# Kernel tuning notes

Hardware: AMD Instinct MI355X
Metric: run time of the kernel (lower is better)

The kernel has to match this reference:

```python
import jax, jax.numpy as jnp
import numpy as np

B, S, D, H = 2, 2048, 1024, 16
HD = D // H  # head_dim = 64


def setup_inputs() -> dict:
    key = jax.random.key(0)
    ks = jax.random.split(key, 12)
    sc = 1.0 / np.sqrt(D)
    return {
        "query": jax.random.normal(ks[0], (B, S, D), jnp.float32),
        "key_": jax.random.normal(ks[1], (B, S, D), jnp.float32),
        "value": jax.random.normal(ks[2], (B, S, D), jnp.float32),
        "mask": jax.random.randint(ks[3], (B, 1, S, S), 0, 2, jnp.int32),
        "Wq": jax.random.normal(ks[4], (D, D), jnp.float32) * sc,
        "bq": jnp.zeros((D,), jnp.float32),
        "Wk": jax.random.normal(ks[5], (D, D), jnp.float32) * sc,
        "bk": jnp.zeros((D,), jnp.float32),
        "Wv": jax.random.normal(ks[6], (D, D), jnp.float32) * sc,
        "bv": jnp.zeros((D,), jnp.float32),
        "Wo": jax.random.normal(ks[7], (D, D), jnp.float32) * sc,
        "bo": jnp.zeros((D,), jnp.float32),
    }


def _split(x):
    # [B, S, D] -> [B, H, S, HD]
    return x.reshape(B, S, H, HD).transpose(0, 2, 1, 3)


def reference(query, key_, value, mask, Wq, bq, Wk, bk, Wv, bv, Wo, bo):
    Q = _split(query @ Wq + bq)
    K = _split(key_ @ Wk + bk)
    V = _split(value @ Wv + bv)
    # scores: [B, H, Sq, Sk]
    scores = jnp.einsum("bhqd,bhkd->bhqk", Q, K) / jnp.sqrt(jnp.float32(HD))
    scores = jnp.where(mask == 0, jnp.float32(-1e9), scores)
    probs = jax.nn.softmax(scores, axis=-1)
    attn = jnp.einsum("bhqk,bhkd->bhqd", probs, V)
    out = attn.transpose(0, 2, 1, 3).reshape(B, S, D)
    return out @ Wo + bo
```

## Files before the change

### kernel.cpp

```cpp
#include <hip/hip_runtime.h>
#include <stdint.h>

typedef _Float16 f16;
typedef _Float16 f16x4 __attribute__((ext_vector_type(4)));
typedef _Float16 f16x8 __attribute__((ext_vector_type(8)));
typedef __fp16 hf16x2 __attribute__((ext_vector_type(2)));
typedef float f32x4 __attribute__((ext_vector_type(4)));
typedef float f32x16 __attribute__((ext_vector_type(16)));
typedef unsigned u32;
typedef unsigned uint2v __attribute__((ext_vector_type(2)));

static constexpr int Bb = 2, Ss = 2048, Dd = 1024, Hh = 16, HDd = 64;
static constexpr int M_ROWS = Bb * Ss;

static constexpr size_t OFF_WT  = 24ull << 20;
static constexpr size_t OFF_QKV = 32ull << 20;
static constexpr size_t OFF_ATT = 56ull << 20;
static constexpr size_t OFF_MB  = 64ull << 20;

__device__ __forceinline__ void gll16(const void* g, void* l) {
  __builtin_amdgcn_global_load_lds((__attribute__((address_space(1))) const void*)g,
                                   (__attribute__((address_space(3))) void*)l, 16, 0, 0);
}

__device__ __forceinline__ int lds_byte(int row, int slot) {
  return row * 128 + (((slot ^ (row & 7)) & 7) << 4);
}

__device__ __forceinline__ float ex2(float x) {
  float r; asm("v_exp_f32 %0, %1" : "=v"(r) : "v"(x)); return r;
}

union H2U { hf16x2 h; u32 u; };

__global__ __launch_bounds__(256) void prep(const int* __restrict__ mask,
                                            unsigned* __restrict__ bits,
                                            const float* __restrict__ wq,
                                            const float* __restrict__ wk,
                                            const float* __restrict__ wv,
                                            const float* __restrict__ wo,
                                            f16* __restrict__ wt) {
  const int bid = blockIdx.x;
  __shared__ float t[32][33];
  if (bid < 32768) {
    size_t i = (size_t)bid * 256 + threadIdx.x;
    int v = mask[i];
    unsigned long long bm = __ballot(v != 0);
    if ((threadIdx.x & 63) == 0) {
      size_t w = i >> 5;
      bits[w]     = (unsigned)bm;
      bits[w + 1] = (unsigned)(bm >> 32);
    }
  } else {
    const int wb = bid - 32768;
    const int z = wb >> 10, by = (wb >> 5) & 31, bx = wb & 31;
    const float* W = z == 0 ? wq : z == 1 ? wk : z == 2 ? wv : wo;
    f16* Wt = wt + (size_t)z * Dd * Dd;
    const int tx = threadIdx.x & 31, ty = threadIdx.x >> 5;
    const int k0 = by * 32, n0 = bx * 32;
    for (int i = 0; i < 32; i += 8) t[ty + i][tx] = W[(size_t)(k0 + ty + i) * Dd + n0 + tx];
    __syncthreads();
    for (int i = 0; i < 32; i += 8) Wt[(size_t)(n0 + ty + i) * Dd + k0 + tx] = (f16)t[tx][ty + i];
  }
}

__global__ __launch_bounds__(256) void gemm_qkv(const float* __restrict__ qin,
                                                const float* __restrict__ kin,
                                                const float* __restrict__ vin,
                                                const f16* __restrict__ Btbase,
                                                const float* __restrict__ b0,
                                                const float* __restrict__ b1,
                                                const float* __restrict__ b2,
                                                f16* __restrict__ Cbase) {
  constexpr int K = Dd, N = Dd;
  const int f = blockIdx.x;
  const int z = f >> 8, i = f & 255;
  const int xg = i & 7, sl = i >> 3;
  const int m0 = (xg * 4 + (sl >> 3)) * 128, n0 = (sl & 7) * 128;
  const float* A = z == 0 ? qin : z == 1 ? kin : vin;
  const f16* Bt = Btbase + (size_t)z * N * K;
  const float* bias = z == 0 ? b0 : z == 1 ? b1 : b2;

  __shared__ char smem[81920];
  const int tid = threadIdx.x, l = tid & 63, w = tid >> 6;
  const int li = l & 15, gq = l >> 4;
  const int wm = (w >> 1) * 64, wn = (w & 1) * 64;
  const int sr = l >> 3, ss = l & 7;
  const int scol = ((ss ^ sr) << 3);

  f32x4 acc[4][4];
  for (int mi = 0; mi < 4; mi++)
    for (int ni = 0; ni < 4; ni++) acc[mi][ni] = f32x4{0.f, 0.f, 0.f, 0.f};

  float4 a0[2][4], a1[2][4];

#pragma unroll
  for (int t = 0; t < 2; t++) {
    const int kt = t * 64;
#pragma unroll
    for (int c = 0; c < 4; c++) {
      int chunk = w * 4 + c, r = chunk * 8 + sr;
      gll16(Bt + (size_t)(n0 + r) * K + kt + scol, smem + 32768 + t * 16384 + chunk * 1024);
      const float* src = A + (size_t)(m0 + r) * K + kt + scol;
      a0[t][c] = *(const float4*)src;
      a1[t][c] = *(const float4*)(src + 4);
    }
  }

#pragma unroll
  for (int t = 0; t < 16; t++) {
    if (t < 15) asm volatile("s_waitcnt vmcnt(12)" ::: "memory");
    else        asm volatile("s_waitcnt vmcnt(0)"  ::: "memory");

    {
      char* bufA = smem + (t & 1) * 16384;
#pragma unroll
      for (int c = 0; c < 4; c++) {
        int chunk = w * 4 + c;
        H2U h0, h1, h2, h3;
        h0.h = __builtin_amdgcn_cvt_pkrtz(a0[t & 1][c].x, a0[t & 1][c].y);
        h1.h = __builtin_amdgcn_cvt_pkrtz(a0[t & 1][c].z, a0[t & 1][c].w);
        h2.h = __builtin_amdgcn_cvt_pkrtz(a1[t & 1][c].x, a1[t & 1][c].y);
        h3.h = __builtin_amdgcn_cvt_pkrtz(a1[t & 1][c].z, a1[t & 1][c].w);
        union { u32 uu[4]; f16x8 v8; } pk;
        pk.uu[0] = h0.u; pk.uu[1] = h1.u; pk.uu[2] = h2.u; pk.uu[3] = h3.u;
        *(f16x8*)(bufA + chunk * 1024 + l * 16) = pk.v8;
      }
    }
    asm volatile("s_waitcnt lgkmcnt(0)" ::: "memory");
    __builtin_amdgcn_s_barrier();

    if (t + 2 < 16) {
      const int tn = t + 2, kn = tn * 64;
#pragma unroll
      for (int c = 0; c < 4; c++) {
        int chunk = w * 4 + c, r = chunk * 8 + sr;
        gll16(Bt + (size_t)(n0 + r) * K + kn + scol,
              smem + 32768 + (tn % 3) * 16384 + chunk * 1024);
        const float* src = A + (size_t)(m0 + r) * K + kn + scol;
        a0[tn & 1][c] = *(const float4*)src;
        a1[tn & 1][c] = *(const float4*)(src + 4);
      }
    }
    __builtin_amdgcn_sched_barrier(0);

    const char* Asc = smem + (t & 1) * 16384;
    const char* Bsc = smem + 32768 + (t % 3) * 16384;
#pragma unroll
    for (int ks = 0; ks < 2; ks++) {
      f16x8 af[4], bf[4];
#pragma unroll
      for (int ii = 0; ii < 4; ii++) {
        af[ii] = *(const f16x8*)(Asc + lds_byte(wm + ii * 16 + li, ks * 4 + gq));
        bf[ii] = *(const f16x8*)(Bsc + lds_byte(wn + ii * 16 + li, ks * 4 + gq));
      }
#pragma unroll
      for (int mi = 0; mi < 4; mi++)
#pragma unroll
        for (int ni = 0; ni < 4; ni++)
          acc[mi][ni] = __builtin_amdgcn_mfma_f32_16x16x32_f16(af[mi], bf[ni], acc[mi][ni], 0, 0, 0);
    }
  }

  const float scl = (z == 0) ? 0.18033688011112042f : 1.0f;
  if (z == 2) {
    f16* Vt = Cbase + (size_t)2 * M_ROWS * N;
#pragma unroll
    for (int mi = 0; mi < 4; mi++)
#pragma unroll
      for (int ni = 0; ni < 4; ni++) {
        const int col = n0 + wn + ni * 16 + li;
        const int r0  = m0 + wm + mi * 16 + gq * 4;
        const int bb_ = r0 >> 11, s = r0 & 2047;
        const float bv = bias[col];
        f16x4 pk;
#pragma unroll
        for (int j = 0; j < 4; j++) pk[j] = (f16)(acc[mi][ni][j] + bv);
        *(f16x4*)(Vt + ((size_t)(bb_ * Hh) << 17) + (size_t)col * Ss + s) = pk;
      }
  } else {
    for (int mi = 0; mi < 4; mi++)
      for (int ni = 0; ni < 4; ni++) {
        const int r0  = m0 + wm + mi * 16 + gq * 4;
        const int col = n0 + wn + ni * 16 + li;
        const float bb = bias[col];
#pragma unroll
        for (int j = 0; j < 4; j++) {
          float val = (acc[mi][ni][j] + bb) * scl;
          Cbase[(size_t)z * M_ROWS * N + (size_t)(r0 + j) * N + col] = (f16)val;
        }
      }
  }
}

__global__ __launch_bounds__(256) void gemm_out(const f16* __restrict__ A,
                                                const f16* __restrict__ Bt,
                                                const float* __restrict__ bias,
                                                float* __restrict__ C) {
  constexpr int K = Dd, N = Dd;
  const int f = blockIdx.x;
  const int xg = f & 7, sl = f >> 3;
  const int m0 = (xg * 4 + (sl >> 3)) * 128, n0 = (sl & 7) * 128;
  __shared__ char smem[65536];
  const int tid = threadIdx.x, l = tid & 63, w = tid >> 6;
  const int li = l & 15, gq = l >> 4;
  const int wm = (w >> 1) * 64, wn = (w & 1) * 64;
  const int sr = l >> 3, ss = l & 7;
  const int scol = ((ss ^ sr) << 3);

  f32x4 acc[4][4];
  for (int mi = 0; mi < 4; mi++)
    for (int ni = 0; ni < 4; ni++) acc[mi][ni] = f32x4{0.f, 0.f, 0.f, 0.f};

#pragma unroll
  for (int c = 0; c < 4; c++) {
    int chunk = w * 4 + c, r = chunk * 8 + sr;
    gll16(A  + (size_t)(m0 + r) * K + scol, smem + chunk * 1024);
    gll16(Bt + (size_t)(n0 + r) * K + scol, smem + 16384 + chunk * 1024);
  }

  int cur = 0;
  for (int it = 0; it < 16; it++) {
    __syncthreads();
    char* Asc = smem + cur * 32768;
    char* Bsc = Asc + 16384;
    if (it < 15) {
      char* Asn = smem + (cur ^ 1) * 32768;
      const int kn = (it + 1) * 64;
#pragma unroll
      for (int c = 0; c < 4; c++) {
        int chunk = w * 4 + c, r = chunk * 8 + sr;
        gll16(A  + (size_t)(m0 + r) * K + kn + scol, Asn + chunk * 1024);
        gll16(Bt + (size_t)(n0 + r) * K + kn + scol, Asn + 16384 + chunk * 1024);
      }
    }
#pragma unroll
    for (int ks = 0; ks < 2; ks++) {
      f16x8 af[4], bf[4];
#pragma unroll
      for (int ii = 0; ii < 4; ii++) {
        af[ii] = *(const f16x8*)(Asc + lds_byte(wm + ii * 16 + li, ks * 4 + gq));
        bf[ii] = *(const f16x8*)(Bsc + lds_byte(wn + ii * 16 + li, ks * 4 + gq));
      }
#pragma unroll
      for (int mi = 0; mi < 4; mi++)
#pragma unroll
        for (int ni = 0; ni < 4; ni++)
          acc[mi][ni] = __builtin_amdgcn_mfma_f32_16x16x32_f16(af[mi], bf[ni], acc[mi][ni], 0, 0, 0);
    }
    cur ^= 1;
  }

  for (int mi = 0; mi < 4; mi++)
    for (int ni = 0; ni < 4; ni++) {
      const int r0  = m0 + wm + mi * 16 + gq * 4;
      const int col = n0 + wn + ni * 16 + li;
      const float bb = bias[col];
#pragma unroll
      for (int j = 0; j < 4; j++)
        C[(size_t)(r0 + j) * N + col] = acc[mi][ni][j] + bb;
    }
}

__global__ __launch_bounds__(512, 4) void attn_fused(const f16* __restrict__ Qp,
                                                     const f16* __restrict__ Kp,
                                                     const f16* __restrict__ Vt,
                                                     const u32* __restrict__ mbits,
                                                     f16* __restrict__ outp) {
  const int flat = blockIdx.x;
  const int xcd = flat & 7, jj = flat >> 3;
  const int qt = jj & 15;
  const int hb = xcd * 4 + (jj >> 4);
  const int h = hb & 15, b = hb >> 4;

  const int tid = threadIdx.x, l = tid & 63, w = tid >> 6;
  const int lo = l & 31, hi = l >> 5;
  const int half = w >> 2, wsub = w & 3;
  const int q0 = qt * 128, wq = wsub * 32;

  __shared__ char smem[65536];
  char* hbase = smem + half * 32768;
  char* Qst = smem + 16384;

  const size_t qkbase = (size_t)b * Ss * Dd + (size_t)h * HDd;
  const f16* Vtb = Vt + (size_t)(b * Hh + h) * HDd * Ss;
  const int sr = l >> 3, ss = l & 7;
  const int scol = ((ss ^ sr) << 3);

  for (int c = 0; c < 2; c++) {
    int chunk = w * 2 + c, r = chunk * 8 + sr;
    gll16(Qp + qkbase + (size_t)(q0 + r) * Dd + scol, Qst + chunk * 1024);
  }
  const int kt0 = half * 16;
  for (int c = 0; c < 2; c++) {
    int chunk = wsub * 2 + c, r = chunk * 8 + sr;
    gll16(Kp + qkbase + (size_t)(kt0 * 64 + r) * Dd + scol, hbase + chunk * 1024);
    gll16(Vtb + (size_t)r * Ss + kt0 * 64 + scol, hbase + 8192 + chunk * 1024);
  }
  __syncthreads();

  f16x8 qf[4];
#pragma unroll
  for (int c = 0; c < 4; c++)
    qf[c] = *(const f16x8*)(Qst + lds_byte(wq + lo, 2 * c + hi));
  __syncthreads();

  f32x16 accO0 = {0}, accO1 = {0};
  float m_run = -1e30f, l_run = 0.f;
  const u32* mrow = mbits + (size_t)(b * Ss + q0 + wq + lo) * 64;

  for (int it = 0; it < 16; it++) {
    const int kt = kt0 + it;
    if (it) __syncthreads();
    char* bufc = hbase + (it & 1) * 16384;
    if (it < 15) {
      char* bufn = hbase + ((it + 1) & 1) * 16384;
      const int k0n = (kt + 1) * 64;
      for (int c = 0; c < 2; c++) {
        int chunk = wsub * 2 + c, r = chunk * 8 + sr;
        gll16(Kp + qkbase + (size_t)(k0n + r) * Dd + scol, bufn + chunk * 1024);
        gll16(Vtb + (size_t)r * Ss + k0n + scol, bufn + 8192 + chunk * 1024);
      }
    }
    const char* Kb = bufc;
    const char* Vb = bufc + 8192;

    f32x16 s0 = {0}, s1 = {0};
    __builtin_amdgcn_s_setprio(1);
#pragma unroll
    for (int c = 0; c < 4; c++) {
      f16x8 kf0 = *(const f16x8*)(Kb + lds_byte(lo, 2 * c + hi));
      f16x8 kf1 = *(const f16x8*)(Kb + lds_byte(32 + lo, 2 * c + hi));
      s0 = __builtin_amdgcn_mfma_f32_32x32x16_f16(kf0, qf[c], s0, 0, 0, 0);
      s1 = __builtin_amdgcn_mfma_f32_32x32x16_f16(kf1, qf[c], s1, 0, 0, 0);
    }
    __builtin_amdgcn_s_setprio(0);

    uint2v mw = *(const uint2v*)(mrow + kt * 2);
    u32 wa = mw.x >> (hi << 2);
    u32 wb = mw.y >> (hi << 2);

    float x0 = fmaxf(s0[0], s1[0]), x1 = fmaxf(s0[1], s1[1]);
    float x2 = fmaxf(s0[2], s1[2]), x3 = fmaxf(s0[3], s1[3]);
#pragma unroll
    for (int r = 4; r < 16; r += 4) {
      x0 = fmaxf(x0, fmaxf(s0[r],     s1[r]));
      x1 = fmaxf(x1, fmaxf(s0[r + 1], s1[r + 1]));
      x2 = fmaxf(x2, fmaxf(s0[r + 2], s1[r + 2]));
      x3 = fmaxf(x3, fmaxf(s0[r + 3], s1[r + 3]));
    }
    float pm = fmaxf(fmaxf(x0, x1), fmaxf(x2, x3));

    float mn;
    if (__all(pm <= m_run + 11.5f)) {
      mn = m_run;
    } else {
      pm = fmaxf(pm, __shfl_xor(pm, 32));
      mn = fmaxf(m_run, pm);
      const float so = ex2(m_run - mn);
      m_run = mn;
      l_run *= so;
      accO0 *= so; accO1 *= so;
    }

    float racc = 0.f;
#pragma unroll
    for (int r = 0; r < 16; r++) {
      const int kk = (r & 3) + 8 * (r >> 2);
      u32 ma = (u32)(((int)(wa << (31 - kk))) >> 31);
      u32 mb = (u32)(((int)(wb << (31 - kk))) >> 31);
      float e0 = __uint_as_float(__float_as_uint(ex2(s0[r] - mn)) & ma);
      float e1 = __uint_as_float(__float_as_uint(ex2(s1[r] - mn)) & mb);
      s0[r] = e0; s1[r] = e1;
      racc += e0 + e1;
    }
    l_run += racc;

    u32 pw[16];
#pragma unroll
    for (int j = 0; j < 8; j++) {
      H2U a, c;
      a.h = __builtin_amdgcn_cvt_pkrtz(s0[2 * j], s0[2 * j + 1]);
      c.h = __builtin_amdgcn_cvt_pkrtz(s1[2 * j], s1[2 * j + 1]);
      pw[j] = a.u; pw[8 + j] = c.u;
    }
#pragma unroll
    for (int c = 0; c < 4; c++) {
      asm volatile("v_permlane32_swap_b32 %0, %1" : "+v"(pw[4 * c]), "+v"(pw[4 * c + 2]));
      asm volatile("v_permlane32_swap_b32 %0, %1" : "+v"(pw[4 * c + 1]), "+v"(pw[4 * c + 3]));
    }

    __builtin_amdgcn_s_setprio(1);
#pragma unroll
    for (int c = 0; c < 4; c++) {
      union { u32 u[4]; f16x8 v; } pu;
      pu.u[0] = pw[4 * c]; pu.u[1] = pw[4 * c + 1];
      pu.u[2] = pw[4 * c + 2]; pu.u[3] = pw[4 * c + 3];
      f16x8 vf0 = *(const f16x8*)(Vb + lds_byte(lo, 2 * c + hi));
      f16x8 vf1 = *(const f16x8*)(Vb + lds_byte(32 + lo, 2 * c + hi));
      accO0 = __builtin_amdgcn_mfma_f32_32x32x16_f16(vf0, pu.v, accO0, 0, 0, 0);
      accO1 = __builtin_amdgcn_mfma_f32_32x32x16_f16(vf1, pu.v, accO1, 0, 0, 0);
    }
    __builtin_amdgcn_s_setprio(0);
  }

  __syncthreads();
  float* mg = (float*)smem;
  if (half == 1) {
    float* p = mg + (size_t)(wsub * 64 + l) * 35;
#pragma unroll
    for (int r = 0; r < 16; r++) { p[r] = accO0[r]; p[16 + r] = accO1[r]; }
    p[32] = m_run; p[33] = l_run;
  }
  __syncthreads();
  if (half == 1) return;

  const float* p = mg + (size_t)(wsub * 64 + l) * 35;
  const float mB = p[32], lB = p[33];
  const float m = fmaxf(m_run, mB);
  const float fA = ex2(m_run - m), fB = ex2(mB - m);
  float lmerged = l_run * fA + lB * fB;
#pragma unroll
  for (int r = 0; r < 16; r++) {
    accO0[r] = accO0[r] * fA + p[r] * fB;
    accO1[r] = accO1[r] * fA + p[16 + r] * fB;
  }
  const float lf = lmerged + __shfl_xor(lmerged, 32);
  const float inv = 1.0f / lf;

  char* Ot = smem + 40960 + wsub * 4096;
#pragma unroll
  for (int j = 0; j < 8; j++) {
    H2U pk;
    pk.h = __builtin_amdgcn_cvt_pkrtz(accO0[2 * j] * inv, accO0[2 * j + 1] * inv);
    int slot = (j >> 1);
    int addr = lo * 128 + (((slot ^ (lo & 7)) & 7) << 4) + 4 * (j & 1) + 8 * hi;
    *(u32*)(Ot + addr) = pk.u;
  }
#pragma unroll
  for (int j = 0; j < 8; j++) {
    H2U pk;
    pk.h = __builtin_amdgcn_cvt_pkrtz(accO1[2 * j] * inv, accO1[2 * j + 1] * inv);
    int slot = (j >> 1) + 4;
    int addr = lo * 128 + (((slot ^ (lo & 7)) & 7) << 4) + 4 * (j & 1) + 8 * hi;
    *(u32*)(Ot + addr) = pk.u;
  }
  asm volatile("s_waitcnt lgkmcnt(0)" ::: "memory");
  {
    const int q = l >> 1, halfq = l & 1;
    f16* gbase = outp + qkbase + (size_t)(q0 + wq + q) * Dd + halfq * 32;
#pragma unroll
    for (int c = 0; c < 4; c++) {
      int byte = q * 128 + ((((halfq * 4 + c) ^ (q & 7)) & 7) << 4);
      f16x8 v = *(const f16x8*)(Ot + byte);
      *(f16x8*)(gbase + c * 8) = v;
    }
  }
}

extern "C" void kernel_launch(void* const* d_in, const int* in_sizes, int n_in,
                              void* d_out, int out_size, void* d_ws, size_t ws_size,
                              hipStream_t stream) {
  const float* query = (const float*)d_in[0];
  const float* key_  = (const float*)d_in[1];
  const float* value = (const float*)d_in[2];
  const int*   mask  = (const int*)d_in[3];
  const float* Wq = (const float*)d_in[4];
  const float* bq = (const float*)d_in[5];
  const float* Wk = (const float*)d_in[6];
  const float* bk = (const float*)d_in[7];
  const float* Wv = (const float*)d_in[8];
  const float* bv = (const float*)d_in[9];
  const float* Wo = (const float*)d_in[10];
  const float* bo = (const float*)d_in[11];

  char* ws = (char*)d_ws;
  f16* Wt  = (f16*)(ws + OFF_WT);
  f16* QKV = (f16*)(ws + OFF_QKV);
  f16* ATT = (f16*)(ws + OFF_ATT);
  unsigned* MB = (unsigned*)(ws + OFF_MB);

  prep<<<dim3(32768 + 4096), 256, 0, stream>>>(mask, MB, Wq, Wk, Wv, Wo, Wt);
  gemm_qkv<<<dim3(768), 256, 0, stream>>>(query, key_, value, Wt, bq, bk, bv, QKV);
  attn_fused<<<dim3(512), 512, 0, stream>>>(QKV, QKV + (size_t)M_ROWS * Dd,
                                            QKV + 2 * (size_t)M_ROWS * Dd, MB, ATT);
  gemm_out<<<dim3(256), 256, 0, stream>>>(ATT, Wt + 3 * (size_t)Dd * Dd, bo, (float*)d_out);
}
```

Baseline: 133.3 us.

## Cut attention LDS to 48KB: Q to registers, single-buffered V

Q fragments are now loaded straight from global memory into registers instead of being staged through LDS. V is single-buffered: it is fetched at the start of each iteration and waited on by a mid-iteration barrier before the PV MFMAs, while K stays double-buffered. This shrinks shared memory from 64KB to 48KB so more workgroups can fit per CU. The cost is an extra barrier per iteration and V load latency that is only partly hidden behind the QK MFMAs and softmax.

```diff
diff --git a/kernel.cpp b/kernel.cpp
--- a/kernel.cpp
+++ b/kernel.cpp
@@ -278,32 +278,24 @@
   const int half = w >> 2, wsub = w & 3;
   const int q0 = qt * 128, wq = wsub * 32;
 
-  __shared__ char smem[65536];
-  char* hbase = smem + half * 32768;
-  char* Qst = smem + 16384;
+  __shared__ char smem[49152];
+  char* hbase = smem + half * 24576;
 
   const size_t qkbase = (size_t)b * Ss * Dd + (size_t)h * HDd;
   const f16* Vtb = Vt + (size_t)(b * Hh + h) * HDd * Ss;
   const int sr = l >> 3, ss = l & 7;
   const int scol = ((ss ^ sr) << 3);
 
-  for (int c = 0; c < 2; c++) {
-    int chunk = w * 2 + c, r = chunk * 8 + sr;
-    gll16(Qp + qkbase + (size_t)(q0 + r) * Dd + scol, Qst + chunk * 1024);
-  }
+  const f16* Qrow = Qp + qkbase + (size_t)(q0 + wq + lo) * Dd;
+  f16x8 qf[4];
+#pragma unroll
+  for (int c = 0; c < 4; c++) qf[c] = *(const f16x8*)(Qrow + 16 * c + 8 * hi);
+
   const int kt0 = half * 16;
   for (int c = 0; c < 2; c++) {
     int chunk = wsub * 2 + c, r = chunk * 8 + sr;
     gll16(Kp + qkbase + (size_t)(kt0 * 64 + r) * Dd + scol, hbase + chunk * 1024);
-    gll16(Vtb + (size_t)r * Ss + kt0 * 64 + scol, hbase + 8192 + chunk * 1024);
-  }
-  __syncthreads();
-
-  f16x8 qf[4];
-#pragma unroll
-  for (int c = 0; c < 4; c++)
-    qf[c] = *(const f16x8*)(Qst + lds_byte(wq + lo, 2 * c + hi));
-  __syncthreads();
+  }
 
   f32x16 accO0 = {0}, accO1 = {0};
   float m_run = -1e30f, l_run = 0.f;
@@ -311,19 +303,22 @@
 
   for (int it = 0; it < 16; it++) {
     const int kt = kt0 + it;
-    if (it) __syncthreads();
-    char* bufc = hbase + (it & 1) * 16384;
+    asm volatile("s_waitcnt vmcnt(0)" ::: "memory");
+    __builtin_amdgcn_s_barrier();
+    __builtin_amdgcn_sched_barrier(0);
+
+    for (int c = 0; c < 2; c++) {
+      int chunk = wsub * 2 + c, r = chunk * 8 + sr;
+      gll16(Vtb + (size_t)r * Ss + kt * 64 + scol, hbase + 16384 + chunk * 1024);
+    }
     if (it < 15) {
-      char* bufn = hbase + ((it + 1) & 1) * 16384;
-      const int k0n = (kt + 1) * 64;
       for (int c = 0; c < 2; c++) {
         int chunk = wsub * 2 + c, r = chunk * 8 + sr;
-        gll16(Kp + qkbase + (size_t)(k0n + r) * Dd + scol, bufn + chunk * 1024);
-        gll16(Vtb + (size_t)r * Ss + k0n + scol, bufn + 8192 + chunk * 1024);
-      }
-    }
-    const char* Kb = bufc;
-    const char* Vb = bufc + 8192;
+        gll16(Kp + qkbase + (size_t)((kt + 1) * 64 + r) * Dd + scol,
+              hbase + ((it + 1) & 1) * 8192 + chunk * 1024);
+      }
+    }
+    const char* Kb = hbase + (it & 1) * 8192;
 
     f32x16 s0 = {0}, s1 = {0};
     __builtin_amdgcn_s_setprio(1);
@@ -390,6 +385,12 @@
       asm volatile("v_permlane32_swap_b32 %0, %1" : "+v"(pw[4 * c + 1]), "+v"(pw[4 * c + 3]));
     }
 
+    if (it < 15) asm volatile("s_waitcnt vmcnt(2)" ::: "memory");
+    else         asm volatile("s_waitcnt vmcnt(0)" ::: "memory");
+    __builtin_amdgcn_s_barrier();
+    __builtin_amdgcn_sched_barrier(0);
+    const char* Vb = hbase + 16384;
+
     __builtin_amdgcn_s_setprio(1);
 #pragma unroll
     for (int c = 0; c < 4; c++) {
@@ -427,8 +428,9 @@
   }
   const float lf = lmerged + __shfl_xor(lmerged, 32);
   const float inv = 1.0f / lf;
-
-  char* Ot = smem + 40960 + wsub * 4096;
+  asm volatile("" ::: "memory");
+
+  char* Ot = smem + wsub * 8960;
 #pragma unroll
   for (int j = 0; j < 8; j++) {
     H2U pk;
```

New measurement: 135.0 us. Within noise of the previous version (+1.3%).
